# Performance work log

Measured on AMD Instinct MI355X. Metric: run time of the kernel, lower is better.

The kernel has to match this reference:

```python
import jax, jax.numpy as jnp
import numpy as np

N_ATOMS, N_BONDS, MAX_NB = 100000, 200000, 6
HIDDEN, DEPTH = 256, 6
ATOM_FDIM, BOND_FDIM = 39, 11


def setup_inputs() -> dict:
    key = jax.random.key(0)
    ks = jax.random.split(key, 6)
    fatoms = jax.random.normal(ks[0], (N_ATOMS, ATOM_FDIM), dtype=jnp.float32)
    fbonds = jax.random.normal(ks[1], (N_BONDS, BOND_FDIM), dtype=jnp.float32)
    # indices into message rows [0, N_BONDS); row 0 is the zero-padding row
    aoutgraph = jax.random.randint(ks[2], (N_ATOMS, MAX_NB), 0, N_BONDS)
    # (x, y) atom-index pairs; entry 0 is padding (unused)
    all_bonds = jax.random.randint(ks[3], (N_BONDS, 2), 0, N_ATOMS)
    # learned params (Linear layers, bias=False): y = x @ W.T
    W_nin = jax.random.normal(ks[4], (HIDDEN, ATOM_FDIM), dtype=jnp.float32) * 0.1
    W_node = jax.random.normal(ks[5], (HIDDEN, HIDDEN + BOND_FDIM), dtype=jnp.float32) * 0.05
    return {"fatoms": fatoms, "fbonds": fbonds, "aoutgraph": aoutgraph,
            "all_bonds": all_bonds, "W_nin": W_nin, "W_node": W_node}


def reference(fatoms, fbonds, aoutgraph, all_bonds, W_nin, W_node):
    # h0 = relu(W_nin @ fatoms); original keeps H_n as [hidden, n_atoms],
    # we keep [n_atoms, hidden] and transpose only at the end (same math).
    h0 = jax.nn.relu(fatoms @ W_nin.T)              # [N, H]
    in_n = all_bonds[1:, 1]                          # target atom of bonds 1..B-1
    zero_row = jnp.zeros((1, HIDDEN), dtype=h0.dtype)
    Hn = h0
    for _ in range(DEPTH):
        # message b = H_n[:, y_b] for b>=1, zero row at b=0, concat bond feats
        atom_msg = jnp.concatenate([zero_row, Hn[in_n]], axis=0)   # [B, H]
        message = jnp.concatenate([atom_msg, fbonds], axis=1)      # [B, H+11]
        # gather neighbor bond messages per atom and sum-aggregate
        nei = message[aoutgraph].sum(axis=1)                       # [N, H+11]
        Hn = jax.nn.relu(h0 + nei @ W_node.T)                      # [N, H]
    return Hn.T                                                    # [H, N] as original
```

## Files before the change

### kernel.cpp

```cpp
#include <hip/hip_runtime.h>

#define N_ATOMS 100000
#define N_BONDS 200000
#define MAX_NB 6
#define HIDDEN 256
#define DEPTH 6
#define ATOM_FDIM 39
#define BOND_FDIM 11
#define WNODE_COLS (HIDDEN + BOND_FDIM)

typedef __attribute__((ext_vector_type(8))) short bf16x8;
typedef __attribute__((ext_vector_type(4))) short s16x4;
typedef __attribute__((ext_vector_type(4))) float f32x4;

__device__ __forceinline__ unsigned short f2bf(float x) {
  unsigned u = __float_as_uint(x);
  unsigned r = (u + 0x7FFFu + ((u >> 16) & 1u)) >> 16;
  return (unsigned short)r;
}
__device__ __forceinline__ float bf2f(unsigned short h) {
  return __uint_as_float(((unsigned)h) << 16);
}
__device__ __forceinline__ void split3(float x, short* s1, short* s2, short* s3) {
  unsigned short h1 = f2bf(x);
  float r1 = x - bf2f(h1);
  unsigned short h2 = f2bf(r1);
  float r2 = r1 - bf2f(h2);
  *s1 = (short)h1;
  *s2 = (short)h2;
  *s3 = (short)f2bf(r2);
}

union U4 { short s[4]; s16x4 v; };

__global__ __launch_bounds__(256) void split_w_kernel(
    const float* __restrict__ W, short* __restrict__ Bsp) {
  int g = blockIdx.x * 256 + threadIdx.x;
  int n = g >> 6;
  int k4 = (g & 63) * 4;
  const float* wp = &W[(size_t)n * WNODE_COLS + k4];
  int o = n * 256 + k4;
#pragma unroll
  for (int j = 0; j < 4; ++j) {
    short a, b, c;
    split3(wp[j], &a, &b, &c);
    Bsp[o + j] = a;
    Bsp[65536 + o + j] = b;
    Bsp[131072 + o + j] = c;
  }
}

__global__ __launch_bounds__(256) void init_kernel(
    const float* __restrict__ fatoms,
    const float* __restrict__ fbonds,
    const int* __restrict__ aoutgraph,
    const float* __restrict__ W_nin,
    const float* __restrict__ W_node,
    float* __restrict__ Hn,
    float* __restrict__ base) {
  __shared__ float Wn_lds[ATOM_FDIM * 256];
  __shared__ float Wf_lds[BOND_FDIM * 256];
  __shared__ float fa_lds[32 * 40];
  __shared__ float fs_lds[32 * 12];
  int tid = threadIdx.x;
  int a0 = blockIdx.x * 32;

  for (int k = 0; k < ATOM_FDIM; ++k)
    Wn_lds[k * 256 + tid] = W_nin[tid * ATOM_FDIM + k];
  for (int k = 0; k < BOND_FDIM; ++k)
    Wf_lds[k * 256 + tid] = W_node[tid * WNODE_COLS + HIDDEN + k];
  {
    int a_l = tid >> 3, j8 = tid & 7;
#pragma unroll
    for (int jj = 0; jj < 5; ++jj) {
      int k = j8 * 5 + jj;
      if (k < ATOM_FDIM)
        fa_lds[a_l * 40 + k] = fatoms[(size_t)(a0 + a_l) * ATOM_FDIM + k];
    }
  }
  for (int i = tid; i < 384; i += 256) {
    int a_l = i / 12, f = i - a_l * 12;
    if (f < BOND_FDIM) {
      float s = 0.f;
#pragma unroll
      for (int nb = 0; nb < MAX_NB; ++nb) {
        int b = aoutgraph[(size_t)(a0 + a_l) * MAX_NB + nb];
        s += fbonds[(size_t)b * BOND_FDIM + f];
      }
      fs_lds[a_l * 12 + f] = s;
    }
  }
  __syncthreads();

  int l = tid & 63, w = tid >> 6;
  f32x4 acc1[8] = {};
  f32x4 acc2[8] = {};
  for (int k = 0; k < ATOM_FDIM; ++k) {
    f32x4 wv = *(const f32x4*)&Wn_lds[k * 256 + l * 4];
#pragma unroll
    for (int ai = 0; ai < 8; ++ai) {
      float av = fa_lds[(w * 8 + ai) * 40 + k];
      acc1[ai] += wv * av;
    }
  }
  for (int k = 0; k < BOND_FDIM; ++k) {
    f32x4 wv = *(const f32x4*)&Wf_lds[k * 256 + l * 4];
#pragma unroll
    for (int ai = 0; ai < 8; ++ai) {
      float av = fs_lds[(w * 8 + ai) * 12 + k];
      acc2[ai] += wv * av;
    }
  }
#pragma unroll
  for (int ai = 0; ai < 8; ++ai) {
    int a_g = a0 + w * 8 + ai;
    size_t off = (size_t)a_g * HIDDEN + l * 4;
    f32x4 h0v, bs;
#pragma unroll
    for (int j = 0; j < 4; ++j) {
      float h0j = fmaxf(acc1[ai][j], 0.f);
      h0v[j] = h0j;
      bs[j] = h0j + acc2[ai][j];
    }
    *(f32x4*)&Hn[off] = h0v;
    *(f32x4*)&base[off] = bs;
  }
}

#define KCH 32
#define AST 40

__global__ __launch_bounds__(256, 3) void fused_kernel(
    const float* __restrict__ Hn_in,
    const float* __restrict__ base,
    const short* __restrict__ Bsp,
    const int* __restrict__ aout,
    const int* __restrict__ bonds,
    float* __restrict__ Hn_out) {
  __shared__ short As[2][3][32 * AST];
  __shared__ int src_lds[192];
  int tid = threadIdx.x;
  int a0 = blockIdx.x * 32;

  if (tid < 192) {
    int a_l = tid / 6, nb = tid - a_l * 6;
    int b = aout[(size_t)(a0 + a_l) * MAX_NB + nb];
    src_lds[tid] = (b != 0) ? bonds[2 * b + 1] : -1;
  }
  __syncthreads();

  int lane = tid & 63, w = tid >> 6;
  int lr = lane & 15, lk = lane >> 4;
  int r_a = tid >> 3, q = tid & 7;

  const char* hb = (const char*)Hn_in;
  unsigned voff[MAX_NB];
  float gw[MAX_NB];
#pragma unroll
  for (int nb = 0; nb < MAX_NB; ++nb) {
    int s = src_lds[r_a * 6 + nb];
    int sr = s >= 0 ? s : 0;
    gw[nb] = s >= 0 ? 1.f : 0.f;
    voff[nb] = (unsigned)((sr * HIDDEN + q * 4) * 4);
  }
  int ao_st = r_a * AST + q * 4;

  f32x4 acc[2][4] = {};

  {
    f32x4 v = {0.f, 0.f, 0.f, 0.f};
#pragma unroll
    for (int nb = 0; nb < MAX_NB; ++nb)
      v += *(const f32x4*)(hb + voff[nb]) * gw[nb];
    U4 t1, t2, t3;
#pragma unroll
    for (int j = 0; j < 4; ++j) split3(v[j], &t1.s[j], &t2.s[j], &t3.s[j]);
    *(s16x4*)&As[0][0][ao_st] = t1.v;
    *(s16x4*)&As[0][1][ao_st] = t2.v;
    *(s16x4*)&As[0][2][ao_st] = t3.v;
  }
  __syncthreads();

#pragma unroll
  for (int c = 0; c < 8; ++c) {
    const int cur = c & 1;
    bf16x8 b0[4], b1[4], b2[4];
#pragma unroll
    for (int n = 0; n < 4; ++n) {
      int bo = (w * 64 + n * 16 + lr) * 256 + c * KCH + lk * 8;
      b0[n] = *(const bf16x8*)&Bsp[bo];
      b1[n] = *(const bf16x8*)&Bsp[65536 + bo];
      b2[n] = *(const bf16x8*)&Bsp[131072 + bo];
    }
    f32x4 ga[MAX_NB];
    if (c < 7) {
#pragma unroll
      for (int nb = 0; nb < MAX_NB; ++nb)
        ga[nb] = *(const f32x4*)(hb + voff[nb] + (c + 1) * KCH * 4);
    }
    __builtin_amdgcn_sched_barrier(0);
    __builtin_amdgcn_s_setprio(1);
#pragma unroll
    for (int m = 0; m < 2; ++m) {
      int ao = (m * 16 + lr) * AST + lk * 8;
      bf16x8 af0 = *(const bf16x8*)&As[cur][0][ao];
      bf16x8 af1 = *(const bf16x8*)&As[cur][1][ao];
      bf16x8 af2 = *(const bf16x8*)&As[cur][2][ao];
#pragma unroll
      for (int n = 0; n < 4; ++n) {
        f32x4 cc = acc[m][n];
        cc = __builtin_amdgcn_mfma_f32_16x16x32_bf16(af0, b0[n], cc, 0, 0, 0);
        cc = __builtin_amdgcn_mfma_f32_16x16x32_bf16(af0, b1[n], cc, 0, 0, 0);
        cc = __builtin_amdgcn_mfma_f32_16x16x32_bf16(af1, b0[n], cc, 0, 0, 0);
        cc = __builtin_amdgcn_mfma_f32_16x16x32_bf16(af1, b1[n], cc, 0, 0, 0);
        cc = __builtin_amdgcn_mfma_f32_16x16x32_bf16(af0, b2[n], cc, 0, 0, 0);
        cc = __builtin_amdgcn_mfma_f32_16x16x32_bf16(af2, b0[n], cc, 0, 0, 0);
        acc[m][n] = cc;
      }
    }
    __builtin_amdgcn_s_setprio(0);
    if (c < 7) {
      f32x4 v = {0.f, 0.f, 0.f, 0.f};
#pragma unroll
      for (int nb = 0; nb < MAX_NB; ++nb) v += ga[nb] * gw[nb];
      U4 t1, t2, t3;
#pragma unroll
      for (int j = 0; j < 4; ++j) split3(v[j], &t1.s[j], &t2.s[j], &t3.s[j]);
      *(s16x4*)&As[cur ^ 1][0][ao_st] = t1.v;
      *(s16x4*)&As[cur ^ 1][1][ao_st] = t2.v;
      *(s16x4*)&As[cur ^ 1][2][ao_st] = t3.v;
      __syncthreads();
    }
  }

#pragma unroll
  for (int m = 0; m < 2; ++m) {
    int row0 = a0 + m * 16 + lk * 4;
#pragma unroll
    for (int n = 0; n < 4; ++n) {
      int col = w * 64 + n * 16 + lr;
#pragma unroll
      for (int r = 0; r < 4; ++r) {
        size_t off = (size_t)(row0 + r) * HIDDEN + col;
        float v = fmaxf(base[off] + acc[m][n][r], 0.f);
        __builtin_nontemporal_store(v, &Hn_out[off]);
      }
    }
  }
}

__global__ __launch_bounds__(256) void transpose_kernel(
    const float* __restrict__ Hn, float* __restrict__ out) {
  __shared__ float tile[64][68];
  int a0 = blockIdx.x * 64, h0 = blockIdx.y * 64;
  int tid = threadIdx.x;
#pragma unroll
  for (int p = 0; p < 2; ++p) {
    int id = tid + p * 256;
    int r = id >> 3, c8 = (id & 7) * 8;
    int ag = a0 + r;
    if (ag > N_ATOMS - 1) ag = N_ATOMS - 1;
    const float* hp = &Hn[(size_t)ag * HIDDEN + h0 + c8];
    *(f32x4*)&tile[r][c8] = *(const f32x4*)hp;
    *(f32x4*)&tile[r][c8 + 4] = *(const f32x4*)(hp + 4);
  }
  __syncthreads();
  int h = tid >> 2, as = (tid & 3) * 16;
  size_t ob = (size_t)(h0 + h) * N_ATOMS + a0 + as;
  if (a0 + 64 <= N_ATOMS) {
#pragma unroll
    for (int q = 0; q < 4; ++q) {
      f32x4 v;
#pragma unroll
      for (int j = 0; j < 4; ++j) v[j] = tile[as + q * 4 + j][h];
      __builtin_nontemporal_store(v, (f32x4*)&out[ob + q * 4]);
    }
  } else {
    for (int j = 0; j < 16; ++j)
      if (a0 + as + j < N_ATOMS)
        __builtin_nontemporal_store(tile[as + j][h], &out[ob + j]);
  }
}

extern "C" void kernel_launch(void* const* d_in, const int* in_sizes, int n_in,
                              void* d_out, int out_size, void* d_ws, size_t ws_size,
                              hipStream_t stream) {
  const float* fatoms = (const float*)d_in[0];
  const float* fbonds = (const float*)d_in[1];
  const int* aoutgraph = (const int*)d_in[2];
  const int* all_bonds = (const int*)d_in[3];
  const float* W_nin = (const float*)d_in[4];
  const float* W_node = (const float*)d_in[5];
  float* out = (float*)d_out;

  const size_t NH = (size_t)N_ATOMS * HIDDEN;
  float* base = (float*)d_ws;
  float* HnA = base + NH;
  short* Bsp = (short*)(HnA + NH);
  float* HnB = out;

  split_w_kernel<<<64, 256, 0, stream>>>(W_node, Bsp);
  init_kernel<<<N_ATOMS / 32, 256, 0, stream>>>(fatoms, fbonds, aoutgraph,
                                                W_nin, W_node, HnA, base);

  const int nblk = N_ATOMS / 32;
  for (int it = 0; it < DEPTH; ++it) {
    const float* in = (it & 1) ? HnB : HnA;
    float* o = (it & 1) ? HnA : HnB;
    fused_kernel<<<nblk, 256, 0, stream>>>(in, base, Bsp, aoutgraph,
                                           all_bonds, o);
  }
  dim3 tgrid((N_ATOMS + 63) / 64, HIDDEN / 64);
  transpose_kernel<<<tgrid, 256, 0, stream>>>(HnA, out);
}
```

Before: 1.443 ms.

## Recompute h0 and bond-feature term in each layer instead of loading base

Drops the precomputed base buffer (h0 plus summed bond features times W_f). Each fused layer kernel now recomputes relu(fatoms·W_nin) and the bond-feature contribution from small inputs, using transposed weight copies made by a new prep kernel, and seeds the accumulator with the result. This removes a 100 MB read of base per layer and its write in init, at the cost of extra FP32 FMAs, fbonds gathers and more LDS per block, which may lower occupancy. The neighbour Hn gather loads are also issued before this compute so their latency can overlap with it.

```diff
diff --git a/kernel.cpp b/kernel.cpp
--- a/kernel.cpp
+++ b/kernel.cpp
@@ -50,80 +50,55 @@
   }
 }
 
+__global__ __launch_bounds__(256) void prep_t_kernel(
+    const float* __restrict__ W_nin, const float* __restrict__ W_node,
+    float* __restrict__ Wn_t, float* __restrict__ Wf_t) {
+  int n = threadIdx.x;
+  for (int k = 0; k < ATOM_FDIM; ++k)
+    Wn_t[k * 256 + n] = W_nin[(size_t)n * ATOM_FDIM + k];
+  for (int k = 0; k < BOND_FDIM; ++k)
+    Wf_t[k * 256 + n] = W_node[(size_t)n * WNODE_COLS + HIDDEN + k];
+}
+
 __global__ __launch_bounds__(256) void init_kernel(
     const float* __restrict__ fatoms,
-    const float* __restrict__ fbonds,
-    const int* __restrict__ aoutgraph,
     const float* __restrict__ W_nin,
-    const float* __restrict__ W_node,
-    float* __restrict__ Hn,
-    float* __restrict__ base) {
+    float* __restrict__ Hn) {
   __shared__ float Wn_lds[ATOM_FDIM * 256];
-  __shared__ float Wf_lds[BOND_FDIM * 256];
-  __shared__ float fa_lds[32 * 40];
-  __shared__ float fs_lds[32 * 12];
+  __shared__ float fa_lds[32 * 41];
   int tid = threadIdx.x;
   int a0 = blockIdx.x * 32;
 
   for (int k = 0; k < ATOM_FDIM; ++k)
     Wn_lds[k * 256 + tid] = W_nin[tid * ATOM_FDIM + k];
-  for (int k = 0; k < BOND_FDIM; ++k)
-    Wf_lds[k * 256 + tid] = W_node[tid * WNODE_COLS + HIDDEN + k];
   {
     int a_l = tid >> 3, j8 = tid & 7;
 #pragma unroll
     for (int jj = 0; jj < 5; ++jj) {
       int k = j8 * 5 + jj;
       if (k < ATOM_FDIM)
-        fa_lds[a_l * 40 + k] = fatoms[(size_t)(a0 + a_l) * ATOM_FDIM + k];
-    }
-  }
-  for (int i = tid; i < 384; i += 256) {
-    int a_l = i / 12, f = i - a_l * 12;
-    if (f < BOND_FDIM) {
-      float s = 0.f;
-#pragma unroll
-      for (int nb = 0; nb < MAX_NB; ++nb) {
-        int b = aoutgraph[(size_t)(a0 + a_l) * MAX_NB + nb];
-        s += fbonds[(size_t)b * BOND_FDIM + f];
-      }
-      fs_lds[a_l * 12 + f] = s;
+        fa_lds[a_l * 41 + k] = fatoms[(size_t)(a0 + a_l) * ATOM_FDIM + k];
     }
   }
   __syncthreads();
 
   int l = tid & 63, w = tid >> 6;
   f32x4 acc1[8] = {};
-  f32x4 acc2[8] = {};
   for (int k = 0; k < ATOM_FDIM; ++k) {
     f32x4 wv = *(const f32x4*)&Wn_lds[k * 256 + l * 4];
 #pragma unroll
     for (int ai = 0; ai < 8; ++ai) {
-      float av = fa_lds[(w * 8 + ai) * 40 + k];
+      float av = fa_lds[(w * 8 + ai) * 41 + k];
       acc1[ai] += wv * av;
     }
   }
-  for (int k = 0; k < BOND_FDIM; ++k) {
-    f32x4 wv = *(const f32x4*)&Wf_lds[k * 256 + l * 4];
-#pragma unroll
-    for (int ai = 0; ai < 8; ++ai) {
-      float av = fs_lds[(w * 8 + ai) * 12 + k];
-      acc2[ai] += wv * av;
-    }
-  }
 #pragma unroll
   for (int ai = 0; ai < 8; ++ai) {
-    int a_g = a0 + w * 8 + ai;
-    size_t off = (size_t)a_g * HIDDEN + l * 4;
-    f32x4 h0v, bs;
-#pragma unroll
-    for (int j = 0; j < 4; ++j) {
-      float h0j = fmaxf(acc1[ai][j], 0.f);
-      h0v[j] = h0j;
-      bs[j] = h0j + acc2[ai][j];
-    }
+    size_t off = (size_t)(a0 + w * 8 + ai) * HIDDEN + l * 4;
+    f32x4 h0v;
+#pragma unroll
+    for (int j = 0; j < 4; ++j) h0v[j] = fmaxf(acc1[ai][j], 0.f);
     *(f32x4*)&Hn[off] = h0v;
-    *(f32x4*)&base[off] = bs;
   }
 }
 
@@ -132,22 +107,48 @@
 
 __global__ __launch_bounds__(256, 3) void fused_kernel(
     const float* __restrict__ Hn_in,
-    const float* __restrict__ base,
     const short* __restrict__ Bsp,
     const int* __restrict__ aout,
     const int* __restrict__ bonds,
+    const float* __restrict__ fatoms,
+    const float* __restrict__ fbonds,
+    const float* __restrict__ Wn_t,
+    const float* __restrict__ Wf_t,
     float* __restrict__ Hn_out) {
   __shared__ short As[2][3][32 * AST];
+  __shared__ int aout_lds[192];
   __shared__ int src_lds[192];
+  __shared__ float fa_lds[32 * 41];
+  __shared__ float fbs_lds[32 * 12];
   int tid = threadIdx.x;
   int a0 = blockIdx.x * 32;
 
   if (tid < 192) {
-    int a_l = tid / 6, nb = tid - a_l * 6;
-    int b = aout[(size_t)(a0 + a_l) * MAX_NB + nb];
+    int b = aout[(size_t)a0 * MAX_NB + tid];
+    aout_lds[tid] = b;
     src_lds[tid] = (b != 0) ? bonds[2 * b + 1] : -1;
   }
-  __syncthreads();
+  {
+    int a_l = tid >> 3, j8 = tid & 7;
+#pragma unroll
+    for (int jj = 0; jj < 5; ++jj) {
+      int k = j8 * 5 + jj;
+      if (k < ATOM_FDIM)
+        fa_lds[a_l * 41 + k] = fatoms[(size_t)(a0 + a_l) * ATOM_FDIM + k];
+    }
+  }
+  __syncthreads();
+
+  for (int i = tid; i < 32 * BOND_FDIM; i += 256) {
+    int a_l = i / BOND_FDIM, f = i - a_l * BOND_FDIM;
+    float s = 0.f;
+#pragma unroll
+    for (int nb = 0; nb < MAX_NB; ++nb) {
+      int b = aout_lds[a_l * MAX_NB + nb];
+      s += fbonds[(size_t)b * BOND_FDIM + f];
+    }
+    fbs_lds[a_l * 12 + f] = s;
+  }
 
   int lane = tid & 63, w = tid >> 6;
   int lr = lane & 15, lk = lane >> 4;
@@ -165,13 +166,61 @@
   }
   int ao_st = r_a * AST + q * 4;
 
+  f32x4 g0[MAX_NB];
+#pragma unroll
+  for (int nb = 0; nb < MAX_NB; ++nb)
+    g0[nb] = *(const f32x4*)(hb + voff[nb]);
+
+  __syncthreads();
+
   f32x4 acc[2][4] = {};
+#pragma unroll 4
+  for (int k = 0; k < ATOM_FDIM; ++k) {
+    float wv[4];
+#pragma unroll
+    for (int n = 0; n < 4; ++n) wv[n] = Wn_t[k * 256 + w * 64 + n * 16 + lr];
+    float fav[2][4];
+#pragma unroll
+    for (int m = 0; m < 2; ++m)
+#pragma unroll
+      for (int r = 0; r < 4; ++r)
+        fav[m][r] = fa_lds[(m * 16 + lk * 4 + r) * 41 + k];
+#pragma unroll
+    for (int m = 0; m < 2; ++m)
+#pragma unroll
+      for (int n = 0; n < 4; ++n)
+#pragma unroll
+        for (int r = 0; r < 4; ++r) acc[m][n][r] += fav[m][r] * wv[n];
+  }
+#pragma unroll
+  for (int m = 0; m < 2; ++m)
+#pragma unroll
+    for (int n = 0; n < 4; ++n)
+#pragma unroll
+      for (int r = 0; r < 4; ++r) acc[m][n][r] = fmaxf(acc[m][n][r], 0.f);
+#pragma unroll
+  for (int k = 0; k < BOND_FDIM; ++k) {
+    float wv[4];
+#pragma unroll
+    for (int n = 0; n < 4; ++n) wv[n] = Wf_t[k * 256 + w * 64 + n * 16 + lr];
+    float fbv[2][4];
+#pragma unroll
+    for (int m = 0; m < 2; ++m)
+#pragma unroll
+      for (int r = 0; r < 4; ++r)
+        fbv[m][r] = fbs_lds[(m * 16 + lk * 4 + r) * 12 + k];
+#pragma unroll
+    for (int m = 0; m < 2; ++m)
+#pragma unroll
+      for (int n = 0; n < 4; ++n)
+#pragma unroll
+        for (int r = 0; r < 4; ++r) acc[m][n][r] += fbv[m][r] * wv[n];
+  }
 
   {
     f32x4 v = {0.f, 0.f, 0.f, 0.f};
 #pragma unroll
-    for (int nb = 0; nb < MAX_NB; ++nb)
-      v += *(const f32x4*)(hb + voff[nb]) * gw[nb];
+    for (int nb = 0; nb < MAX_NB; ++nb) v += g0[nb] * gw[nb];
     U4 t1, t2, t3;
 #pragma unroll
     for (int j = 0; j < 4; ++j) split3(v[j], &t1.s[j], &t2.s[j], &t3.s[j]);
@@ -242,8 +291,7 @@
 #pragma unroll
       for (int r = 0; r < 4; ++r) {
         size_t off = (size_t)(row0 + r) * HIDDEN + col;
-        float v = fmaxf(base[off] + acc[m][n][r], 0.f);
-        __builtin_nontemporal_store(v, &Hn_out[off]);
+        Hn_out[off] = fmaxf(acc[m][n][r], 0.f);
       }
     }
   }
@@ -294,21 +342,22 @@
   float* out = (float*)d_out;
 
   const size_t NH = (size_t)N_ATOMS * HIDDEN;
-  float* base = (float*)d_ws;
-  float* HnA = base + NH;
+  float* HnA = (float*)d_ws;
   short* Bsp = (short*)(HnA + NH);
+  float* Wn_t = (float*)(Bsp + 3 * 65536);
+  float* Wf_t = Wn_t + ATOM_FDIM * 256;
   float* HnB = out;
 
   split_w_kernel<<<64, 256, 0, stream>>>(W_node, Bsp);
-  init_kernel<<<N_ATOMS / 32, 256, 0, stream>>>(fatoms, fbonds, aoutgraph,
-                                                W_nin, W_node, HnA, base);
+  prep_t_kernel<<<1, 256, 0, stream>>>(W_nin, W_node, Wn_t, Wf_t);
+  init_kernel<<<N_ATOMS / 32, 256, 0, stream>>>(fatoms, W_nin, HnA);
 
   const int nblk = N_ATOMS / 32;
   for (int it = 0; it < DEPTH; ++it) {
     const float* in = (it & 1) ? HnB : HnA;
     float* o = (it & 1) ? HnA : HnB;
-    fused_kernel<<<nblk, 256, 0, stream>>>(in, base, Bsp, aoutgraph,
-                                           all_bonds, o);
+    fused_kernel<<<nblk, 256, 0, stream>>>(in, Bsp, aoutgraph, all_bonds,
+                                           fatoms, fbonds, Wn_t, Wf_t, o);
   }
   dim3 tgrid((N_ATOMS + 63) / 64, HIDDEN / 64);
   transpose_kernel<<<tgrid, 256, 0, stream>>>(HnA, out);
```

New measurement: 1.871 ms. 29.6% more time.
